# Kernel optimization log

Hardware: AMD Instinct MI355X
Metric: run time of the kernel (lower is better)

The kernel has to match this reference:

```python
import jax, jax.numpy as jnp
import numpy as np

B, S, E, H = 4, 512, 512, 8
DH = E // H
HID = max(16, E // 4)  # sr_ratio=4
ALPHA = 0.1
EPS_SAFE = 0.05  # eps=1e-6 clamped to [0.05, 0.8]


def _xavier(k, shape):
    fan_out, fan_in = shape[0], shape[1]
    lim = (6.0 / (fan_in + fan_out)) ** 0.5
    return jax.random.uniform(k, shape, minval=-lim, maxval=lim, dtype=jnp.float32)


def setup_inputs() -> dict:
    key = jax.random.key(0)
    ks = jax.random.split(key, 8)
    return {
        "x": jax.random.normal(ks[0], (B, S, E), dtype=jnp.float32),
        "wq": _xavier(ks[1], (E, E)), "bq": jnp.zeros((E,), jnp.float32),
        "wk": _xavier(ks[2], (E, E)), "bk": jnp.zeros((E,), jnp.float32),
        "wv": _xavier(ks[3], (E, E)), "bv": jnp.zeros((E,), jnp.float32),
        "wo": _xavier(ks[4], (E, E)), "bo": jnp.zeros((E,), jnp.float32),
        # sr_conv1: Conv2d(1, HID, 1) -> weight [HID,1,1,1] == vector [HID]
        "w1": _xavier(ks[5], (HID, 1)).reshape(HID), "b1": jnp.zeros((HID,), jnp.float32),
        # sr_conv2: Conv2d(HID, 1, 1) -> weight [1,HID,1,1] == vector [HID]
        "w2": _xavier(ks[6], (1, HID)).reshape(HID), "b2": jnp.zeros((), jnp.float32),
    }


def _autopoietic_transform(scores, w1, b1, w2, b2):
    # scores: [B, H, S, S]
    scores = jnp.clip(jnp.nan_to_num(scores, nan=0.0, posinf=10.0, neginf=-10.0), -15.0, 15.0)
    mean_attn = scores.mean(axis=1)  # mean over heads -> [B, S, S]

    scaled = jnp.clip(jnp.clip(mean_attn, -8.0, 8.0) * EPS_SAFE, -10.0, 10.0)
    # conv1x1 (1 -> HID): broadcastmul; clamp + relu; conv1x1 (HID -> 1)
    hid = scaled[:, None, :, :] * w1[None, :, None, None] + b1[None, :, None, None]  # [B,HID,S,S]
    hid = jax.nn.relu(jnp.clip(hid, -5.0, 5.0))
    auto = jnp.einsum('bhij,h->bij', hid, w2) + b2  # [B,S,S]
    auto = jnp.clip(auto, -5.0, 5.0)

    # Taylor expansion with clamp, then sigmoid smoothing
    taylor = jnp.clip(1.0 + 0.05 * (auto * 50.0), 0.5, 1.5)
    sig = jax.nn.sigmoid(taylor)

    # fuzzy probability via entropy of softmax of mean attention
    p = jax.nn.softmax(jnp.clip(mean_attn, -10.0, 10.0), axis=-1)
    Hent = -p * jnp.log(p + 1e-6)
    Fm = jax.nn.softmax(3.0 * Hent, axis=-1)

    t = sig * Fm

    # energy (Frobenius-norm) balancing per batch
    e_o = jnp.sqrt((mean_attn ** 2).sum(axis=(1, 2))) + 1e-4
    e_t = jnp.sqrt((t ** 2).sum(axis=(1, 2))) + 1e-4
    gamma = jnp.clip(e_o / e_t, 0.8, 1.2)[:, None, None]
    t = gamma * t

    # dynamic std matching
    t_mean = t.mean(axis=(1, 2), keepdims=True)
    o_mean = mean_attn.mean(axis=(1, 2), keepdims=True)
    t_std = jnp.sqrt(jnp.clip(((t - t_mean) ** 2).mean(axis=(1, 2), keepdims=True), 0.01, None))
    o_std = jnp.sqrt(jnp.clip(((mean_attn - o_mean) ** 2).mean(axis=(1, 2), keepdims=True), 0.01, None))
    gdyn = jnp.clip(o_std / t_std, 0.8, 1.2)
    t = o_mean + gdyn * (t - t_mean)

    # residual blend of transformed map back into per-head scores (alpha=0.1), final clamp
    return jnp.clip(scores + ALPHA * t[:, None, :, :], -15.0, 15.0)


def reference(x, wq, bq, wk, bk, wv, bv, wo, bo, w1, b1, w2, b2):
    scaling = DH ** -0.5
    q = (jnp.einsum('bse,oe->bso', x, wq) + bq).reshape(B, S, H, DH).transpose(0, 2, 1, 3) * scaling
    k = (jnp.einsum('bse,oe->bso', x, wk) + bk).reshape(B, S, H, DH).transpose(0, 2, 1, 3)
    v = (jnp.einsum('bse,oe->bso', x, wv) + bv).reshape(B, S, H, DH).transpose(0, 2, 1, 3)
    scores = jnp.einsum('bhqd,bhkd->bhqk', q, k)  # [B,H,S,S]
    scores = _autopoietic_transform(scores, w1, b1, w2, b2)
    attn = jax.nn.softmax(scores, axis=-1)
    out = jnp.einsum('bhqk,bhkd->bhqd', attn, v).transpose(0, 2, 1, 3).reshape(B, S, E)
    return jnp.einsum('bse,oe->bso', out, wo) + bo
```

## Files before the change

kernel.cpp:

```cpp
#include <hip/hip_runtime.h>
#include <math.h>

#define BATCH 4
#define SEQ   512
#define EMB   512
#define NH    8
#define DHD   64
#define HIDN  128
#define ALPHA 0.1f
#define EPSS  0.05f

#define LUTN  2048
#define XMIN  (-0.4f)
#define XSTEP (0.8f / LUTN)

typedef __attribute__((ext_vector_type(8))) short  bf16x8;
typedef __attribute__((ext_vector_type(4))) float  f32x4;
#define MFMA(a,b,c) __builtin_amdgcn_mfma_f32_16x16x32_bf16((a),(b),(c),0,0,0)

__device__ __forceinline__ unsigned short f2bf(float f) {
    union { float f; unsigned u; } v; v.f = f;
    unsigned r = v.u + 0x7fffu + ((v.u >> 16) & 1u);
    return (unsigned short)(r >> 16);
}
__device__ __forceinline__ float bf2f(unsigned short h) {
    union { unsigned u; float f; } v; v.u = ((unsigned)h) << 16;
    return v.f;
}

__device__ __forceinline__ void async_lds16(const unsigned short* g, unsigned short* l) {
    __builtin_amdgcn_global_load_lds(
        (const __attribute__((address_space(1))) void*)g,
        (__attribute__((address_space(3))) void*)l, 16, 0, 0);
}

template<int KSTEPS, int UN>
__device__ __forceinline__ void gemm_core(
    const unsigned short* __restrict__ A, const unsigned short* __restrict__ B,
    int m0, int n0, unsigned short* sA, unsigned short* sB, f32x4 acc[2][4])
{
    const int K = KSTEPS * 32;
    const int tid = threadIdx.x, w = tid >> 6, lane = tid & 63;
    const int quad = lane >> 4, r = lane & 15;
    const int wm = w >> 1, wn = w & 1;
    const int lrow = lane >> 2, lc = lane & 3;
    const int sc = lc ^ (lrow & 3);
    const unsigned short* ag  = A + (long)(m0 + w * 16 + lrow) * K + sc * 8;
    const unsigned short* bg0 = B + (long)(n0 + w * 16 + lrow) * K + sc * 8;
    const unsigned short* bg1 = (UN == 4)
        ? B + (long)(n0 + (w + 4) * 16 + lrow) * K + sc * 8 : (const unsigned short*)0;
    unsigned short* dA  = sA + w * 512;
    unsigned short* dB0 = sB + w * 512;
    unsigned short* dB1 = sB + (w + 4) * 512;
    const int cs = quad ^ (r & 3);

    for (int s = 0; s < KSTEPS; s++) {
        const int k0 = s * 32;
        async_lds16(ag + k0, dA);
        async_lds16(bg0 + k0, dB0);
        if (UN == 4) async_lds16(bg1 + k0, dB1);
        __syncthreads();
        bf16x8 af[2], bf[4];
        #pragma unroll
        for (int t = 0; t < 2; t++)
            af[t] = *(const bf16x8*)(sA + (wm * 32 + t * 16 + r) * 32 + cs * 8);
        #pragma unroll
        for (int u = 0; u < UN; u++)
            bf[u] = *(const bf16x8*)(sB + (wn * UN * 16 + u * 16 + r) * 32 + cs * 8);
        #pragma unroll
        for (int t = 0; t < 2; t++)
            #pragma unroll
            for (int u = 0; u < UN; u++)
                acc[t][u] = MFMA(af[t], bf[u], acc[t][u]);
        __syncthreads();
    }
}

__global__ __launch_bounds__(256) void gemm_qkv(
    const unsigned short* __restrict__ x_ext, const unsigned short* __restrict__ w_ext,
    const float* __restrict__ bq, const float* __restrict__ bk, const float* __restrict__ bv,
    unsigned short* __restrict__ q_ext, unsigned short* __restrict__ k_ext,
    unsigned short* __restrict__ vT)
{
    __shared__ __align__(16) unsigned short sA[64 * 32];
    __shared__ __align__(16) unsigned short sB[64 * 32];
    __shared__ float sC[64 * 68];

    const int m0 = blockIdx.y * 64, n0 = blockIdx.x * 64;
    f32x4 acc[2][4] = {};
    gemm_core<48, 2>(x_ext, w_ext, m0, n0, sA, sB, acc);

    const int tid = threadIdx.x, w = tid >> 6, lane = tid & 63;
    const int quad = lane >> 4, r = lane & 15;
    const int wm = w >> 1, wn = w & 1;
    #pragma unroll
    for (int t = 0; t < 2; t++)
        #pragma unroll
        for (int u = 0; u < 2; u++)
            #pragma unroll
            for (int g = 0; g < 4; g++)
                sC[(wm * 32 + t * 16 + quad * 4 + g) * 68 + wn * 32 + u * 16 + r] = acc[t][u][g];
    __syncthreads();

    const int which = n0 >> 9;
    const int n0l = n0 & 511;
    const int h0 = n0l >> 6;
    const int b = m0 >> 9, s0 = m0 & 511;

    if (which < 2) {
        const float scl = (which == 0) ? 0.125f : 1.0f;
        const float* bias = (which == 0) ? bq : bk;
        unsigned* dst = (unsigned*)((which == 0) ? q_ext : k_ext);
        #pragma unroll
        for (int seg = 0; seg < 3; seg++) {
            const bool lo = (which == 0) ? (seg == 1) : (seg == 2);
            #pragma unroll
            for (int it = 0; it < 8; it++) {
                const int idx = it * 256 + tid;
                const int sl = idx >> 5;
                const int jc = idx & 31;
                const int nc = jc * 2;
                float v0 = (sC[sl * 68 + nc]     + bias[n0l + nc])     * scl;
                float v1 = (sC[sl * 68 + nc + 1] + bias[n0l + nc + 1]) * scl;
                unsigned short a0 = f2bf(v0), a1 = f2bf(v1);
                if (lo) { a0 = f2bf(v0 - bf2f(a0)); a1 = f2bf(v1 - bf2f(a1)); }
                const long orow = (long)(b * NH + h0) * SEQ + s0 + sl;
                dst[orow * 96 + seg * 32 + jc] = (unsigned)a0 | ((unsigned)a1 << 16);
            }
        }
    } else {
        unsigned* dst = (unsigned*)vT;
        #pragma unroll
        for (int it = 0; it < 8; it++) {
            const int idx = it * 256 + tid;
            const int d = idx >> 5;
            const int jc = idx & 31;
            const int sl = jc * 2;
            const float bvv = bv[n0l + d];
            const float v0 = sC[sl * 68 + d] + bvv;
            const float v1 = sC[(sl + 1) * 68 + d] + bvv;
            const long orow = (long)(b * NH + h0) * DHD + d;
            dst[orow * 256 + (s0 >> 1) + jc] = (unsigned)f2bf(v0) | ((unsigned)f2bf(v1) << 16);
        }
    }
}

__global__ __launch_bounds__(256) void gemm_scores(
    const unsigned short* __restrict__ q_ext, const unsigned short* __restrict__ k_ext,
    float* __restrict__ scores)
{
    __shared__ __align__(16) unsigned short sA[64 * 32];
    __shared__ __align__(16) unsigned short sB[128 * 32];
    const int z = blockIdx.z;
    const int m0 = blockIdx.y * 64, n0 = blockIdx.x * 128;
    f32x4 acc[2][4] = {};
    gemm_core<6, 4>(q_ext + (long)z * SEQ * 192, k_ext + (long)z * SEQ * 192,
                    m0, n0, sA, sB, acc);
    float* C = scores + (long)z * SEQ * SEQ;
    const int tid = threadIdx.x, w = tid >> 6, lane = tid & 63;
    const int quad = lane >> 4, r = lane & 15;
    const int wm = w >> 1, wn = w & 1;
    #pragma unroll
    for (int t = 0; t < 2; t++)
        #pragma unroll
        for (int u = 0; u < 4; u++)
            #pragma unroll
            for (int g = 0; g < 4; g++) {
                const int m = m0 + wm * 32 + t * 16 + quad * 4 + g;
                const int n = n0 + wn * 64 + u * 16 + r;
                C[(long)m * SEQ + n] = fminf(fmaxf(acc[t][u][g], -15.f), 15.f);
            }
}

__global__ __launch_bounds__(256) void gemm_proj(
    const unsigned short* __restrict__ otmp, const unsigned short* __restrict__ woh,
    const float* __restrict__ bo, float* __restrict__ out)
{
    __shared__ __align__(16) unsigned short sA[64 * 32];
    __shared__ __align__(16) unsigned short sB[64 * 32];
    const int m0 = blockIdx.y * 64, n0 = blockIdx.x * 64;
    f32x4 acc[2][4] = {};
    gemm_core<16, 2>(otmp, woh, m0, n0, sA, sB, acc);
    const int tid = threadIdx.x, w = tid >> 6, lane = tid & 63;
    const int quad = lane >> 4, r = lane & 15;
    const int wm = w >> 1, wn = w & 1;
    #pragma unroll
    for (int t = 0; t < 2; t++)
        #pragma unroll
        for (int u = 0; u < 2; u++)
            #pragma unroll
            for (int g = 0; g < 4; g++) {
                const int m = m0 + wm * 32 + t * 16 + quad * 4 + g;
                const int n = n0 + wn * 32 + u * 16 + r;
                out[(long)m * EMB + n] = acc[t][u][g] + bo[n];
            }
}

__device__ __forceinline__ float blockReduceSum(float v, float* sred) {
    #pragma unroll
    for (int o = 32; o > 0; o >>= 1) v += __shfl_down(v, o);
    __syncthreads();
    if ((threadIdx.x & 63) == 0) sred[threadIdx.x >> 6] = v;
    __syncthreads();
    return (sred[0] + sred[1]) + (sred[2] + sred[3]);
}
__device__ __forceinline__ float blockReduceMax(float v, float* sred) {
    #pragma unroll
    for (int o = 32; o > 0; o >>= 1) v = fmaxf(v, __shfl_down(v, o));
    __syncthreads();
    if ((threadIdx.x & 63) == 0) sred[threadIdx.x >> 6] = v;
    __syncthreads();
    return fmaxf(fmaxf(sred[0], sred[1]), fmaxf(sred[2], sred[3]));
}

__global__ __launch_bounds__(256) void prep_kernel(
    const float* __restrict__ x,
    const float* __restrict__ wq, const float* __restrict__ wk,
    const float* __restrict__ wv, const float* __restrict__ wo,
    const float* __restrict__ w1, const float* __restrict__ b1,
    const float* __restrict__ w2, const float* __restrict__ b2,
    unsigned short* __restrict__ x_ext, unsigned short* __restrict__ w_ext,
    unsigned short* __restrict__ woh, float* __restrict__ lut)
{
    const int blk = blockIdx.x;
    if (blk < 9) {
        const int i = blk * 256 + threadIdx.x;
        if (i > LUTN) return;
        const float xv = XMIN + i * XSTEP;
        float a = 0.f;
        for (int h = 0; h < HIDN; h++) {
            float hv = xv * w1[h] + b1[h];
            hv = fminf(fmaxf(hv, -5.f), 5.f);
            hv = fmaxf(hv, 0.f);
            a += hv * w2[h];
        }
        a += b2[0];
        a = fminf(fmaxf(a, -5.f), 5.f);
        const float taylor = fminf(fmaxf(1.f + 2.5f * a, 0.5f), 1.5f);
        lut[i] = 1.f / (1.f + expf(-taylor));
        return;
    }
    const int i = (blk - 9) * 256 + threadIdx.x;
    if (i < 1048576) {
        const int m = i >> 9, k = i & 511;
        const float v = x[i];
        const unsigned short h = f2bf(v), l = f2bf(v - bf2f(h));
        const long bb = (long)m * 1536 + k;
        x_ext[bb] = h; x_ext[bb + 512] = l; x_ext[bb + 1024] = h;
    } else if (i < 1835008) {
        const int j = i - 1048576;
        const int n = j >> 9, k = j & 511;
        const float v = (j < 262144) ? wq[j] : (j < 524288 ? wk[j - 262144] : wv[j - 524288]);
        const unsigned short h = f2bf(v), l = f2bf(v - bf2f(h));
        const long bb = (long)n * 1536 + k;
        w_ext[bb] = h; w_ext[bb + 512] = h; w_ext[bb + 1024] = l;
    } else {
        const int j = i - 1835008;
        woh[j] = f2bf(wo[j]);
    }
}

__global__ __launch_bounds__(256) void transform_kernel(
    const float* __restrict__ scores,
    const float* __restrict__ lut,
    float* __restrict__ t0,
    float4* __restrict__ partials)
{
    const int r = blockIdx.x;
    const int b = r >> 9, i = r & 511;
    const int tid = threadIdx.x;

    __shared__ float slut[LUTN + 1];
    __shared__ float sred[4];

    for (int u = tid; u <= LUTN; u += 256) slut[u] = lut[u];

    const float* base = scores + (((long)(b * NH)) * SEQ + i) * SEQ;

    float mv[2], sigv[2], mclip[2];
    float lmax = -1e30f;
    __syncthreads();
    #pragma unroll
    for (int u = 0; u < 2; u++) {
        const int j = tid + u * 256;
        float s = 0.f;
        #pragma unroll
        for (int h = 0; h < NH; h++) s += base[(long)h * SEQ * SEQ + j];
        const float m = s * (1.0f / NH);
        mv[u] = m;
        const float x = fminf(fmaxf(m, -8.f), 8.f) * EPSS;
        float t = (x - XMIN) * (1.0f / XSTEP);
        int idx = (int)t;
        idx = idx < 0 ? 0 : (idx > LUTN - 1 ? LUTN - 1 : idx);
        const float frac = t - (float)idx;
        const float l0 = slut[idx], l1 = slut[idx + 1];
        sigv[u] = l0 + frac * (l1 - l0);
        const float mc = fminf(fmaxf(m, -10.f), 10.f);
        mclip[u] = mc;
        lmax = fmaxf(lmax, mc);
    }

    const float rmax = blockReduceMax(lmax, sred);
    float ex[2], lsum = 0.f;
    #pragma unroll
    for (int u = 0; u < 2; u++) { ex[u] = expf(mclip[u] - rmax); lsum += ex[u]; }
    const float rsum = blockReduceSum(lsum, sred);
    const float inv = 1.f / rsum;

    float hent[2], lmax2 = -1e30f;
    #pragma unroll
    for (int u = 0; u < 2; u++) {
        const float p = ex[u] * inv;
        const float he = -p * logf(p + 1e-6f);
        hent[u] = 3.f * he;
        lmax2 = fmaxf(lmax2, hent[u]);
    }
    const float rmax2 = blockReduceMax(lmax2, sred);
    float ex2[2], lsum2 = 0.f;
    #pragma unroll
    for (int u = 0; u < 2; u++) { ex2[u] = expf(hent[u] - rmax2); lsum2 += ex2[u]; }
    const float rsum2 = blockReduceSum(lsum2, sred);
    const float inv2 = 1.f / rsum2;

    float s_m = 0.f, s_m2 = 0.f, s_t = 0.f, s_t2 = 0.f;
    #pragma unroll
    for (int u = 0; u < 2; u++) {
        const int j = tid + u * 256;
        const float Fm = ex2[u] * inv2;
        const float tv = sigv[u] * Fm;
        t0[((long)b * SEQ + i) * SEQ + j] = tv;
        s_m += mv[u]; s_m2 += mv[u] * mv[u];
        s_t += tv;    s_t2 += tv * tv;
    }
    s_m  = blockReduceSum(s_m,  sred);
    s_m2 = blockReduceSum(s_m2, sred);
    s_t  = blockReduceSum(s_t,  sred);
    s_t2 = blockReduceSum(s_t2, sred);
    if (tid == 0) {
        partials[r] = make_float4(s_m, s_m2, s_t, s_t2);
    }
}

__global__ __launch_bounds__(256) void softmax_attnv(
    const float* __restrict__ scores,
    const float* __restrict__ t0,
    const float4* __restrict__ partials,
    const unsigned short* __restrict__ vT,
    unsigned short* __restrict__ otmp)
{
    __shared__ __align__(16) unsigned short attnS[32 * 520];
    __shared__ __align__(16) unsigned short sB[64 * 32];
    __shared__ float sC[32 * 66];
    __shared__ float sred[4];

    const int m0 = blockIdx.x * 32;
    const int z  = blockIdx.y;
    const int b  = z >> 3, h = z & 7;
    const int tid = threadIdx.x, wv = tid >> 6, lane = tid & 63;

    const float4 p0 = partials[b * SEQ + tid];
    const float4 p1 = partials[b * SEQ + tid + 256];
    float sm  = blockReduceSum(p0.x + p1.x, sred);
    float sm2 = blockReduceSum(p0.y + p1.y, sred);
    float st  = blockReduceSum(p0.z + p1.z, sred);
    float st2 = blockReduceSum(p0.w + p1.w, sred);
    const float n = (float)SEQ * (float)SEQ;
    const float gamma = fminf(fmaxf((sqrtf(sm2) + 1e-4f) / (sqrtf(st2) + 1e-4f), 0.8f), 1.2f);
    const float o_mean = sm / n, t0m = st / n;
    const float o_std = sqrtf(fmaxf(fmaxf(sm2 / n - o_mean * o_mean, 0.f), 0.01f));
    const float t_std = sqrtf(fmaxf(gamma * gamma * fmaxf(st2 / n - t0m * t0m, 0.f), 0.01f));
    const float gdyn = fminf(fmaxf(o_std / t_std, 0.8f), 1.2f);
    const float c1 = gdyn * gamma;
    const float c0 = o_mean - c1 * t0m;

    const int j0 = lane * 8;
    for (int it = 0; it < 8; it++) {
        const int rowl = it * 4 + wv;
        const float* srow = scores + ((long)z * SEQ + m0 + rowl) * SEQ + j0;
        const float* trow = t0 + ((long)b * SEQ + m0 + rowl) * SEQ + j0;
        const float4 s0 = ((const float4*)srow)[0], s1 = ((const float4*)srow)[1];
        const float4 tt0 = ((const float4*)trow)[0], tt1 = ((const float4*)trow)[1];
        float sv[8] = { s0.x, s0.y, s0.z, s0.w, s1.x, s1.y, s1.z, s1.w };
        const float tvv[8] = { tt0.x, tt0.y, tt0.z, tt0.w, tt1.x, tt1.y, tt1.z, tt1.w };
        float lmax = -1e30f;
        #pragma unroll
        for (int u = 0; u < 8; u++) {
            float s = sv[u] + ALPHA * (c0 + c1 * tvv[u]);
            s = fminf(fmaxf(s, -15.f), 15.f);
            sv[u] = s;
            lmax = fmaxf(lmax, s);
        }
        #pragma unroll
        for (int o = 32; o > 0; o >>= 1) lmax = fmaxf(lmax, __shfl_down(lmax, o));
        lmax = __shfl(lmax, 0);
        float lsum = 0.f;
        #pragma unroll
        for (int u = 0; u < 8; u++) { sv[u] = expf(sv[u] - lmax); lsum += sv[u]; }
        #pragma unroll
        for (int o = 32; o > 0; o >>= 1) lsum += __shfl_down(lsum, o);
        lsum = __shfl(lsum, 0);
        const float inv = 1.f / lsum;
        bf16x8 pk;
        #pragma unroll
        for (int u = 0; u < 8; u++) pk[u] = (short)f2bf(sv[u] * inv);
        *(bf16x8*)(attnS + rowl * 520 + j0) = pk;
    }
    __syncthreads();

    const int quad = lane >> 4, r = lane & 15;
    const int wm = wv >> 1, wn = wv & 1;
    const int lrow = lane >> 2, lc = lane & 3;
    const int sc = lc ^ (lrow & 3);
    const int cs = quad ^ (r & 3);
    const unsigned short* bg = vT + (long)z * DHD * SEQ + (long)(wv * 16 + lrow) * SEQ + sc * 8;
    unsigned short* dB = sB + wv * 512;
    f32x4 acc[2] = {};
    for (int kc = 0; kc < 16; kc++) {
        async_lds16(bg + kc * 32, dB);
        __syncthreads();
        const bf16x8 a = *(const bf16x8*)(attnS + (wm * 16 + r) * 520 + kc * 32 + quad * 8);
        const bf16x8 b0 = *(const bf16x8*)(sB + (wn * 32 + r) * 32 + cs * 8);
        const bf16x8 b1 = *(const bf16x8*)(sB + (wn * 32 + 16 + r) * 32 + cs * 8);
        acc[0] = MFMA(a, b0, acc[0]);
        acc[1] = MFMA(a, b1, acc[1]);
        __syncthreads();
    }

    #pragma unroll
    for (int u = 0; u < 2; u++)
        #pragma unroll
        for (int g = 0; g < 4; g++)
            sC[(wm * 16 + quad * 4 + g) * 66 + wn * 32 + u * 16 + r] = acc[u][g];
    __syncthreads();
    unsigned* dst = (unsigned*)otmp;
    #pragma unroll
    for (int it = 0; it < 4; it++) {
        const int idx = it * 256 + tid;
        const int sr = idx >> 5, jc = idx & 31;
        const float v0 = sC[sr * 66 + jc * 2], v1 = sC[sr * 66 + jc * 2 + 1];
        dst[((long)(b * SEQ + m0 + sr)) * 256 + h * 32 + jc] =
            (unsigned)f2bf(v0) | ((unsigned)f2bf(v1) << 16);
    }
}

extern "C" void kernel_launch(void* const* d_in, const int* in_sizes, int n_in,
                              void* d_out, int out_size, void* d_ws, size_t ws_size,
                              hipStream_t stream) {
    const float* x  = (const float*)d_in[0];
    const float* wq = (const float*)d_in[1];
    const float* bq = (const float*)d_in[2];
    const float* wk = (const float*)d_in[3];
    const float* bk = (const float*)d_in[4];
    const float* wv = (const float*)d_in[5];
    const float* bv = (const float*)d_in[6];
    const float* wo = (const float*)d_in[7];
    const float* bo = (const float*)d_in[8];
    const float* w1 = (const float*)d_in[9];
    const float* b1 = (const float*)d_in[10];
    const float* w2 = (const float*)d_in[11];
    const float* b2 = (const float*)d_in[12];
    float* out = (float*)d_out;

    char* wsb = (char*)d_ws;
    float*  scores   = (float*)wsb;
    float*  t0       = scores + 8388608;
    float4* partials = (float4*)(t0 + 1048576);
    float*  lutbuf   = (float*)(partials + 2048);
    unsigned short* u16 = (unsigned short*)(wsb + (40u << 20));
    unsigned short* x_ext = u16;
    unsigned short* w_ext = x_ext + 3145728;
    unsigned short* q_ext = w_ext + 2359296;
    unsigned short* k_ext = q_ext + 3145728;
    unsigned short* vT    = k_ext + 3145728;
    unsigned short* otmp  = vT + 1048576;
    unsigned short* woh   = otmp + 1048576;

    prep_kernel<<<dim3(9 + 8192), dim3(256), 0, stream>>>(
        x, wq, wk, wv, wo, w1, b1, w2, b2, x_ext, w_ext, woh, lutbuf);

    gemm_qkv<<<dim3(24, 32), dim3(256), 0, stream>>>(
        x_ext, w_ext, bq, bk, bv, q_ext, k_ext, vT);

    gemm_scores<<<dim3(4, 8, 32), dim3(256), 0, stream>>>(q_ext, k_ext, scores);

    transform_kernel<<<dim3(BATCH * SEQ), dim3(256), 0, stream>>>(
        scores, lutbuf, t0, partials);

    softmax_attnv<<<dim3(16, 32), dim3(256), 0, stream>>>(
        scores, t0, partials, vT, otmp);

    gemm_proj<<<dim3(8, 32), dim3(256), 0, stream>>>(otmp, woh, bo, out);
}
```

Before: 164.4 us.

## Store scores and transform map in fp16 and widen GEMM K-tiles to 64

Scores and the per-batch transform map now go to workspace as fp16 instead of fp32, which halves the traffic of the dominant intermediates read by the transform and softmax kernels. The scores GEMM stages its tile through LDS so it can issue 16-byte coalesced stores. All GEMM cores switch to 64-wide K steps with an 8-way XOR swizzle, halving the number of barrier-separated iterations. The projection GEMM uses 32-row tiles so more blocks run. fp16 storage adds rounding error to scores in [-15,15] and to the small transform values.

```diff
diff --git a/kernel.cpp b/kernel.cpp
--- a/kernel.cpp
+++ b/kernel.cpp
@@ -27,6 +27,12 @@
     union { unsigned u; float f; } v; v.u = ((unsigned)h) << 16;
     return v.f;
 }
+__device__ __forceinline__ float f16tof(unsigned short h) {
+    union { unsigned short s; _Float16 f; } v; v.s = h; return (float)v.f;
+}
+__device__ __forceinline__ unsigned short ftof16(float f) {
+    union { unsigned short s; _Float16 f; } v; v.f = (_Float16)f; return v.s;
+}
 
 __device__ __forceinline__ void async_lds16(const unsigned short* g, unsigned short* l) {
     __builtin_amdgcn_global_load_lds(
@@ -34,44 +40,61 @@
         (__attribute__((address_space(3))) void*)l, 16, 0, 0);
 }
 
-template<int KSTEPS, int UN>
-__device__ __forceinline__ void gemm_core(
+template<int KS, int UN, int MT>
+__device__ __forceinline__ void gemm_core64(
     const unsigned short* __restrict__ A, const unsigned short* __restrict__ B,
-    int m0, int n0, unsigned short* sA, unsigned short* sB, f32x4 acc[2][4])
-{
-    const int K = KSTEPS * 32;
+    int m0, int n0, unsigned short* sA, unsigned short* sB, f32x4 (&acc)[2][4])
+{
+    const int K = KS * 64;
     const int tid = threadIdx.x, w = tid >> 6, lane = tid & 63;
     const int quad = lane >> 4, r = lane & 15;
     const int wm = w >> 1, wn = w & 1;
-    const int lrow = lane >> 2, lc = lane & 3;
-    const int sc = lc ^ (lrow & 3);
-    const unsigned short* ag  = A + (long)(m0 + w * 16 + lrow) * K + sc * 8;
-    const unsigned short* bg0 = B + (long)(n0 + w * 16 + lrow) * K + sc * 8;
-    const unsigned short* bg1 = (UN == 4)
-        ? B + (long)(n0 + (w + 4) * 16 + lrow) * K + sc * 8 : (const unsigned short*)0;
-    unsigned short* dA  = sA + w * 512;
-    unsigned short* dB0 = sB + w * 512;
-    unsigned short* dB1 = sB + (w + 4) * 512;
-    const int cs = quad ^ (r & 3);
-
-    for (int s = 0; s < KSTEPS; s++) {
-        const int k0 = s * 32;
-        async_lds16(ag + k0, dA);
-        async_lds16(bg0 + k0, dB0);
-        if (UN == 4) async_lds16(bg1 + k0, dB1);
+    const int lrow = lane >> 3, lc = lane & 7;
+    const int sc = lc ^ lrow;
+    constexpr int AF = MT / 32;
+    constexpr int NB = UN * 32 / 32;
+
+    const unsigned short* ag[2]; unsigned short* dAu[2];
+    #pragma unroll
+    for (int c = 0; c < AF; c++) {
+        const int rb = w * (8 * AF) + c * 8;
+        ag[c]  = A + (long)(m0 + rb + lrow) * K + sc * 8;
+        dAu[c] = sA + rb * 64;
+    }
+    const unsigned short* bg[4]; unsigned short* dBu[4];
+    #pragma unroll
+    for (int c = 0; c < NB; c++) {
+        const int rb = w * (8 * NB) + c * 8;
+        bg[c]  = B + (long)(n0 + rb + lrow) * K + sc * 8;
+        dBu[c] = sB + rb * 64;
+    }
+
+    for (int s = 0; s < KS; s++) {
+        const int k0 = s * 64;
+        #pragma unroll
+        for (int c = 0; c < AF; c++) async_lds16(ag[c] + k0, dAu[c]);
+        #pragma unroll
+        for (int c = 0; c < NB; c++) async_lds16(bg[c] + k0, dBu[c]);
         __syncthreads();
-        bf16x8 af[2], bf[4];
-        #pragma unroll
-        for (int t = 0; t < 2; t++)
-            af[t] = *(const bf16x8*)(sA + (wm * 32 + t * 16 + r) * 32 + cs * 8);
-        #pragma unroll
-        for (int u = 0; u < UN; u++)
-            bf[u] = *(const bf16x8*)(sB + (wn * UN * 16 + u * 16 + r) * 32 + cs * 8);
-        #pragma unroll
-        for (int t = 0; t < 2; t++)
-            #pragma unroll
-            for (int u = 0; u < UN; u++)
-                acc[t][u] = MFMA(af[t], bf[u], acc[t][u]);
+        #pragma unroll
+        for (int kc = 0; kc < 2; kc++) {
+            bf16x8 af[2], bfr[4];
+            #pragma unroll
+            for (int t = 0; t < AF; t++) {
+                const int row = wm * (16 * AF) + t * 16 + r;
+                af[t] = *(const bf16x8*)(sA + row * 64 + ((kc * 4 + quad) ^ (row & 7)) * 8);
+            }
+            #pragma unroll
+            for (int u = 0; u < UN; u++) {
+                const int row = wn * (16 * UN) + u * 16 + r;
+                bfr[u] = *(const bf16x8*)(sB + row * 64 + ((kc * 4 + quad) ^ (row & 7)) * 8);
+            }
+            #pragma unroll
+            for (int t = 0; t < AF; t++)
+                #pragma unroll
+                for (int u = 0; u < UN; u++)
+                    acc[t][u] = MFMA(af[t], bfr[u], acc[t][u]);
+        }
         __syncthreads();
     }
 }
@@ -82,13 +105,13 @@
     unsigned short* __restrict__ q_ext, unsigned short* __restrict__ k_ext,
     unsigned short* __restrict__ vT)
 {
-    __shared__ __align__(16) unsigned short sA[64 * 32];
-    __shared__ __align__(16) unsigned short sB[64 * 32];
+    __shared__ __align__(16) unsigned short sA[64 * 64];
+    __shared__ __align__(16) unsigned short sB[64 * 64];
     __shared__ float sC[64 * 68];
 
     const int m0 = blockIdx.y * 64, n0 = blockIdx.x * 64;
     f32x4 acc[2][4] = {};
-    gemm_core<48, 2>(x_ext, w_ext, m0, n0, sA, sB, acc);
+    gemm_core64<24, 2, 64>(x_ext, w_ext, m0, n0, sA, sB, acc);
 
     const int tid = threadIdx.x, w = tid >> 6, lane = tid & 63;
     const int quad = lane >> 4, r = lane & 15;
@@ -147,53 +170,60 @@
 
 __global__ __launch_bounds__(256) void gemm_scores(
     const unsigned short* __restrict__ q_ext, const unsigned short* __restrict__ k_ext,
-    float* __restrict__ scores)
-{
-    __shared__ __align__(16) unsigned short sA[64 * 32];
-    __shared__ __align__(16) unsigned short sB[128 * 32];
+    unsigned short* __restrict__ scoresH)
+{
+    __shared__ __align__(16) unsigned short sA[64 * 64];
+    __shared__ __align__(16) unsigned short sB[128 * 64];
     const int z = blockIdx.z;
     const int m0 = blockIdx.y * 64, n0 = blockIdx.x * 128;
     f32x4 acc[2][4] = {};
-    gemm_core<6, 4>(q_ext + (long)z * SEQ * 192, k_ext + (long)z * SEQ * 192,
-                    m0, n0, sA, sB, acc);
-    float* C = scores + (long)z * SEQ * SEQ;
+    gemm_core64<3, 4, 64>(q_ext + (long)z * SEQ * 192, k_ext + (long)z * SEQ * 192,
+                          m0, n0, sA, sB, acc);
+
     const int tid = threadIdx.x, w = tid >> 6, lane = tid & 63;
     const int quad = lane >> 4, r = lane & 15;
     const int wm = w >> 1, wn = w & 1;
+    unsigned short* hC = sB;
     #pragma unroll
     for (int t = 0; t < 2; t++)
         #pragma unroll
         for (int u = 0; u < 4; u++)
             #pragma unroll
             for (int g = 0; g < 4; g++) {
-                const int m = m0 + wm * 32 + t * 16 + quad * 4 + g;
-                const int n = n0 + wn * 64 + u * 16 + r;
-                C[(long)m * SEQ + n] = fminf(fmaxf(acc[t][u][g], -15.f), 15.f);
+                const int ml = wm * 32 + t * 16 + quad * 4 + g;
+                const int nl = wn * 64 + u * 16 + r;
+                hC[ml * 128 + nl] = ftof16(fminf(fmaxf(acc[t][u][g], -15.f), 15.f));
             }
+    __syncthreads();
+    #pragma unroll
+    for (int it = 0; it < 4; it++) {
+        const int id = it * 256 + tid;
+        const int ml = id >> 4, ch = id & 15;
+        *(uint4*)(scoresH + ((long)z * SEQ + m0 + ml) * SEQ + n0 + ch * 8) =
+            *(const uint4*)(hC + ml * 128 + ch * 8);
+    }
 }
 
 __global__ __launch_bounds__(256) void gemm_proj(
     const unsigned short* __restrict__ otmp, const unsigned short* __restrict__ woh,
     const float* __restrict__ bo, float* __restrict__ out)
 {
-    __shared__ __align__(16) unsigned short sA[64 * 32];
-    __shared__ __align__(16) unsigned short sB[64 * 32];
-    const int m0 = blockIdx.y * 64, n0 = blockIdx.x * 64;
+    __shared__ __align__(16) unsigned short sA[32 * 64];
+    __shared__ __align__(16) unsigned short sB[64 * 64];
+    const int m0 = blockIdx.y * 32, n0 = blockIdx.x * 64;
     f32x4 acc[2][4] = {};
-    gemm_core<16, 2>(otmp, woh, m0, n0, sA, sB, acc);
+    gemm_core64<8, 2, 32>(otmp, woh, m0, n0, sA, sB, acc);
     const int tid = threadIdx.x, w = tid >> 6, lane = tid & 63;
     const int quad = lane >> 4, r = lane & 15;
     const int wm = w >> 1, wn = w & 1;
     #pragma unroll
-    for (int t = 0; t < 2; t++)
-        #pragma unroll
-        for (int u = 0; u < 2; u++)
-            #pragma unroll
-            for (int g = 0; g < 4; g++) {
-                const int m = m0 + wm * 32 + t * 16 + quad * 4 + g;
-                const int n = n0 + wn * 32 + u * 16 + r;
-                out[(long)m * EMB + n] = acc[t][u][g] + bo[n];
-            }
+    for (int u = 0; u < 2; u++)
+        #pragma unroll
+        for (int g = 0; g < 4; g++) {
+            const int m = m0 + wm * 16 + quad * 4 + g;
+            const int n = n0 + wn * 32 + u * 16 + r;
+            out[(long)m * EMB + n] = acc[0][u][g] + bo[n];
+        }
 }
 
 __device__ __forceinline__ float blockReduceSum(float v, float* sred) {
@@ -261,13 +291,13 @@
 }
 
 __global__ __launch_bounds__(256) void transform_kernel(
-    const float* __restrict__ scores,
+    const unsigned short* __restrict__ scoresH,
     const float* __restrict__ lut,
-    float* __restrict__ t0,
+    unsigned short* __restrict__ t0H,
     float4* __restrict__ partials)
 {
-    const int r = blockIdx.x;
-    const int b = r >> 9, i = r & 511;
+    const int rr = blockIdx.x;
+    const int b = rr >> 9, i = rr & 511;
     const int tid = threadIdx.x;
 
     __shared__ float slut[LUTN + 1];
@@ -275,19 +305,23 @@
 
     for (int u = tid; u <= LUTN; u += 256) slut[u] = lut[u];
 
-    const float* base = scores + (((long)(b * NH)) * SEQ + i) * SEQ;
-
-    float mv[2], sigv[2], mclip[2];
+    const unsigned* baseU =
+        (const unsigned*)(scoresH + (((long)(b * NH)) * SEQ + i) * SEQ) + tid;
+    float s0 = 0.f, s1 = 0.f;
+    #pragma unroll
+    for (int h = 0; h < NH; h++) {
+        const unsigned pv = baseU[h * (SEQ * SEQ / 2)];
+        s0 += f16tof((unsigned short)pv);
+        s1 += f16tof((unsigned short)(pv >> 16));
+    }
+    float mv[2] = { s0 * 0.125f, s1 * 0.125f };
+    __syncthreads();
+
+    float sigv[2], mclip[2];
     float lmax = -1e30f;
-    __syncthreads();
     #pragma unroll
     for (int u = 0; u < 2; u++) {
-        const int j = tid + u * 256;
-        float s = 0.f;
-        #pragma unroll
-        for (int h = 0; h < NH; h++) s += base[(long)h * SEQ * SEQ + j];
-        const float m = s * (1.0f / NH);
-        mv[u] = m;
+        const float m = mv[u];
         const float x = fminf(fmaxf(m, -8.f), 8.f) * EPSS;
         float t = (x - XMIN) * (1.0f / XSTEP);
         int idx = (int)t;
@@ -322,34 +356,28 @@
     const float rsum2 = blockReduceSum(lsum2, sred);
     const float inv2 = 1.f / rsum2;
 
-    float s_m = 0.f, s_m2 = 0.f, s_t = 0.f, s_t2 = 0.f;
-    #pragma unroll
-    for (int u = 0; u < 2; u++) {
-        const int j = tid + u * 256;
-        const float Fm = ex2[u] * inv2;
-        const float tv = sigv[u] * Fm;
-        t0[((long)b * SEQ + i) * SEQ + j] = tv;
-        s_m += mv[u]; s_m2 += mv[u] * mv[u];
-        s_t += tv;    s_t2 += tv * tv;
-    }
-    s_m  = blockReduceSum(s_m,  sred);
-    s_m2 = blockReduceSum(s_m2, sred);
-    s_t  = blockReduceSum(s_t,  sred);
-    s_t2 = blockReduceSum(s_t2, sred);
-    if (tid == 0) {
-        partials[r] = make_float4(s_m, s_m2, s_t, s_t2);
-    }
+    float tv[2];
+    #pragma unroll
+    for (int u = 0; u < 2; u++) tv[u] = sigv[u] * (ex2[u] * inv2);
+    ((unsigned*)t0H)[((long)b * SEQ + i) * (SEQ / 2) + tid] =
+        (unsigned)ftof16(tv[0]) | ((unsigned)ftof16(tv[1]) << 16);
+
+    float s_m  = blockReduceSum(mv[0] + mv[1], sred);
+    float s_m2 = blockReduceSum(mv[0] * mv[0] + mv[1] * mv[1], sred);
+    float s_t  = blockReduceSum(tv[0] + tv[1], sred);
+    float s_t2 = blockReduceSum(tv[0] * tv[0] + tv[1] * tv[1], sred);
+    if (tid == 0) partials[rr] = make_float4(s_m, s_m2, s_t, s_t2);
 }
 
 __global__ __launch_bounds__(256) void softmax_attnv(
-    const float* __restrict__ scores,
-    const float* __restrict__ t0,
+    const unsigned short* __restrict__ scoresH,
+    const unsigned short* __restrict__ t0H,
     const float4* __restrict__ partials,
     const unsigned short* __restrict__ vT,
     unsigned short* __restrict__ otmp)
 {
     __shared__ __align__(16) unsigned short attnS[32 * 520];
-    __shared__ __align__(16) unsigned short sB[64 * 32];
+    __shared__ __align__(16) unsigned short sB[64 * 64];
     __shared__ float sC[32 * 66];
     __shared__ float sred[4];
 
@@ -376,16 +404,14 @@
     const int j0 = lane * 8;
     for (int it = 0; it < 8; it++) {
         const int rowl = it * 4 + wv;
-        const float* srow = scores + ((long)z * SEQ + m0 + rowl) * SEQ + j0;
-        const float* trow = t0 + ((long)b * SEQ + m0 + rowl) * SEQ + j0;
-        const float4 s0 = ((const float4*)srow)[0], s1 = ((const float4*)srow)[1];
-        const float4 tt0 = ((const float4*)trow)[0], tt1 = ((const float4*)trow)[1];
-        float sv[8] = { s0.x, s0.y, s0.z, s0.w, s1.x, s1.y, s1.z, s1.w };
-        const float tvv[8] = { tt0.x, tt0.y, tt0.z, tt0.w, tt1.x, tt1.y, tt1.z, tt1.w };
+        const bf16x8 sr = *(const bf16x8*)(scoresH + ((long)z * SEQ + m0 + rowl) * SEQ + j0);
+        const bf16x8 tr = *(const bf16x8*)(t0H + ((long)b * SEQ + m0 + rowl) * SEQ + j0);
+        float sv[8];
         float lmax = -1e30f;
         #pragma unroll
         for (int u = 0; u < 8; u++) {
-            float s = sv[u] + ALPHA * (c0 + c1 * tvv[u]);
+            float s = f16tof((unsigned short)sr[u])
+                    + ALPHA * (c0 + c1 * f16tof((unsigned short)tr[u]));
             s = fminf(fmaxf(s, -15.f), 15.f);
             sv[u] = s;
             lmax = fmaxf(lmax, s);
@@ -409,20 +435,28 @@
 
     const int quad = lane >> 4, r = lane & 15;
     const int wm = wv >> 1, wn = wv & 1;
-    const int lrow = lane >> 2, lc = lane & 3;
-    const int sc = lc ^ (lrow & 3);
-    const int cs = quad ^ (r & 3);
-    const unsigned short* bg = vT + (long)z * DHD * SEQ + (long)(wv * 16 + lrow) * SEQ + sc * 8;
-    unsigned short* dB = sB + wv * 512;
+    const int lrow = lane >> 3, lc = lane & 7;
+    const int sc = lc ^ lrow;
+    const unsigned short* bg0 = vT + (long)z * DHD * SEQ + (long)(wv * 16 + lrow) * SEQ + sc * 8;
+    const unsigned short* bg1 = bg0 + 8 * SEQ;
+    unsigned short* dB0 = sB + (wv * 16) * 64;
+    unsigned short* dB1 = sB + (wv * 16 + 8) * 64;
     f32x4 acc[2] = {};
-    for (int kc = 0; kc < 16; kc++) {
-        async_lds16(bg + kc * 32, dB);
+    for (int s = 0; s < 8; s++) {
+        const int k0 = s * 64;
+        async_lds16(bg0 + k0, dB0);
+        async_lds16(bg1 + k0, dB1);
         __syncthreads();
-        const bf16x8 a = *(const bf16x8*)(attnS + (wm * 16 + r) * 520 + kc * 32 + quad * 8);
-        const bf16x8 b0 = *(const bf16x8*)(sB + (wn * 32 + r) * 32 + cs * 8);
-        const bf16x8 b1 = *(const bf16x8*)(sB + (wn * 32 + 16 + r) * 32 + cs * 8);
-        acc[0] = MFMA(a, b0, acc[0]);
-        acc[1] = MFMA(a, b1, acc[1]);
+        #pragma unroll
+        for (int kc = 0; kc < 2; kc++) {
+            const bf16x8 a = *(const bf16x8*)(attnS + (wm * 16 + r) * 520 + k0 + kc * 32 + quad * 8);
+            #pragma unroll
+            for (int u = 0; u < 2; u++) {
+                const int row = wn * 32 + u * 16 + r;
+                const bf16x8 bb = *(const bf16x8*)(sB + row * 64 + ((kc * 4 + quad) ^ (row & 7)) * 8);
+                acc[u] = MFMA(a, bb, acc[u]);
+            }
+        }
         __syncthreads();
     }
 
@@ -436,9 +470,9 @@
     #pragma unroll
     for (int it = 0; it < 4; it++) {
         const int idx = it * 256 + tid;
-        const int sr = idx >> 5, jc = idx & 31;
-        const float v0 = sC[sr * 66 + jc * 2], v1 = sC[sr * 66 + jc * 2 + 1];
-        dst[((long)(b * SEQ + m0 + sr)) * 256 + h * 32 + jc] =
+        const int sr2 = idx >> 5, jc = idx & 31;
+        const float v0 = sC[sr2 * 66 + jc * 2], v1 = sC[sr2 * 66 + jc * 2 + 1];
+        dst[((long)(b * SEQ + m0 + sr2)) * 256 + h * 32 + jc] =
             (unsigned)f2bf(v0) | ((unsigned)f2bf(v1) << 16);
     }
 }
@@ -462,11 +496,11 @@
     float* out = (float*)d_out;
 
     char* wsb = (char*)d_ws;
-    float*  scores   = (float*)wsb;
-    float*  t0       = scores + 8388608;
-    float4* partials = (float4*)(t0 + 1048576);
+    unsigned short* scoresH = (unsigned short*)wsb;
+    unsigned short* t0H     = scoresH + 8388608;
+    float4* partials = (float4*)(t0H + 1048576);
     float*  lutbuf   = (float*)(partials + 2048);
-    unsigned short* u16 = (unsigned short*)(wsb + (40u << 20));
+    unsigned short* u16 = (unsigned short*)(wsb + (20u << 20));
     unsigned short* x_ext = u16;
     unsigned short* w_ext = x_ext + 3145728;
     unsigned short* q_ext = w_ext + 2359296;
@@ -481,13 +515,13 @@
     gemm_qkv<<<dim3(24, 32), dim3(256), 0, stream>>>(
         x_ext, w_ext, bq, bk, bv, q_ext, k_ext, vT);
 
-    gemm_scores<<<dim3(4, 8, 32), dim3(256), 0, stream>>>(q_ext, k_ext, scores);
+    gemm_scores<<<dim3(4, 8, 32), dim3(256), 0, stream>>>(q_ext, k_ext, scoresH);
 
     transform_kernel<<<dim3(BATCH * SEQ), dim3(256), 0, stream>>>(
-        scores, lutbuf, t0, partials);
+        scoresH, lutbuf, t0H, partials);
 
     softmax_attnv<<<dim3(16, 32), dim3(256), 0, stream>>>(
-        scores, t0, partials, vT, otmp);
-
-    gemm_proj<<<dim3(8, 32), dim3(256), 0, stream>>>(otmp, woh, bo, out);
-}
+        scoresH, t0H, partials, vT, otmp);
+
+    gemm_proj<<<dim3(8, 64), dim3(256), 0, stream>>>(otmp, woh, bo, out);
+}
```

New measurement: 148.6 us. 9.6% less time.
